# Performance work log

Hardware: AMD Instinct MI355X
Metric: run time of the kernel (lower is better)

The kernel has to match this reference:

```python
import jax, jax.numpy as jnp
import numpy as np

B, C, T, K = 16, 512, 2048, 64

def setup_inputs() -> dict:
    key = jax.random.key(0)
    k1, k2, k3 = jax.random.split(key, 3)
    v = jax.random.normal(k1, (B, C, T), dtype=jnp.float32)
    # 1x1 Conv1d weights == linear maps over channel dim
    Wk = jax.random.normal(k2, (K, C), dtype=jnp.float32) * 0.02
    bk = jnp.zeros((K,), dtype=jnp.float32)
    Wq = jax.random.normal(k3, (K, C), dtype=jnp.float32) * 0.02
    bq = jnp.zeros((K,), dtype=jnp.float32)
    gamma = jnp.ones((), dtype=jnp.float32)
    return {"v": v, "Wk": Wk, "bk": bk, "Wq": Wq, "bq": bq, "gamma": gamma}

def reference(v, Wk, bk, Wq, bq, gamma):
    # k, q: (B, K, T) via 1x1 conv = channel-wise linear
    k = jnp.einsum('kc,bct->bkt', Wk, v) + bk[None, :, None]
    q = jnp.einsum('kc,bct->bkt', Wq, v) + bq[None, :, None]
    # original: e1[b,d,i,j]=q[b,d,j], e2[b,d,i,j]=k[b,d,i]; sum over d
    # -> s[b,i,j] = sum_d k[b,d,i] * q[b,d,j]  (avoid materializing B,K,T,T)
    s = jnp.einsum('bdi,bdj->bij', k, q)  # (B, T, T)
    a = jax.nn.softmax(s, axis=1)          # softmax over dim=1 (the i axis)
    att = jnp.einsum('bct,btj->bcj', v, a)  # bmm(v, a)
    return v + gamma * att
```

## Files before the change

### kernel.cpp

```cpp
#include <hip/hip_runtime.h>

#define Bc 16
#define Cc 512
#define Tc 2048
#define QT 128
#define KT 64
#define NT 32
#define LTS 66

typedef __attribute__((ext_vector_type(8)))  short short8;
typedef __attribute__((ext_vector_type(4)))  float f32x4;
typedef __attribute__((ext_vector_type(16))) float f32x16;
typedef unsigned short u16;

static __device__ __forceinline__ u16 f2bf(float x) {
  unsigned u = __float_as_uint(x);
  u += 0x7FFF + ((u >> 16) & 1);
  return (u16)(u >> 16);
}

static __device__ __forceinline__ unsigned cvt_pk_bf16(float lo, float hi) {
  unsigned r;
  asm("v_cvt_pk_bf16_f32 %0, %1, %2" : "=v"(r) : "v"(lo), "v"(hi));
  return r;
}

static __device__ __forceinline__ void gload_lds16(const u16* gsrc, u16* ldst) {
  __builtin_amdgcn_global_load_lds(
      (const __attribute__((address_space(1))) unsigned int*)gsrc,
      (__attribute__((address_space(3))) unsigned int*)ldst,
      16, 0, 0);
}

static __device__ __forceinline__ void block_sync_lds() {
  __builtin_amdgcn_sched_barrier(0);
  asm volatile("s_waitcnt lgkmcnt(0)" ::: "memory");
  __builtin_amdgcn_s_barrier();
  __builtin_amdgcn_sched_barrier(0);
}

static __device__ __forceinline__ void block_sync_vm4() {
  __builtin_amdgcn_sched_barrier(0);
  asm volatile("s_waitcnt vmcnt(4) lgkmcnt(0)" ::: "memory");
  __builtin_amdgcn_s_barrier();
  __builtin_amdgcn_sched_barrier(0);
}

__global__ __launch_bounds__(256) void prep_kernel(
    const float* __restrict__ Wk, const float* __restrict__ Wq,
    const float* __restrict__ bk, const float* __restrict__ bq,
    u16* __restrict__ Wbf, float* __restrict__ bkq)
{
  int idx  = blockIdx.x * 256 + threadIdx.x;
  int base = idx * 4;
  if (base < 128 * Cc) {
    int ch = base >> 9;
    int c  = base & (Cc - 1);
    const float* src = (ch < 64) ? (Wk + (size_t)ch * Cc + c)
                                 : (Wq + (size_t)(ch - 64) * Cc + c);
    f32x4 w = *reinterpret_cast<const f32x4*>(src);
    uint2 o;
    o.x = (unsigned)f2bf(w[0]) | ((unsigned)f2bf(w[1]) << 16);
    o.y = (unsigned)f2bf(w[2]) | ((unsigned)f2bf(w[3]) << 16);
    *reinterpret_cast<uint2*>(Wbf + base) = o;
  }
  if (idx < 128) bkq[idx] = (idx < 64) ? bk[idx] : bq[idx - 64];
}

__global__ __launch_bounds__(256) void kqv_kernel(
    const float* __restrict__ v, const u16* __restrict__ Wbf,
    const float* __restrict__ bkq, u16* __restrict__ kq, u16* __restrict__ vbf)
{
  __shared__ u16 LDSt[2][64][LTS];
  const int b   = blockIdx.y;
  const int t0  = blockIdx.x * 64;
  const int tid = threadIdx.x;
  const int lane = tid & 63;
  const int w    = tid >> 6;
  const int l15  = lane & 15;
  const int lg   = lane >> 4;

  f32x4 acc[8];
  #pragma unroll
  for (int mt = 0; mt < 8; ++mt) acc[mt] = f32x4{0.f, 0.f, 0.f, 0.f};

  const float* vb = v + (size_t)b * Cc * Tc + t0;
  float x[16];
  #pragma unroll
  for (int r = 0; r < 16; ++r) x[r] = vb[(size_t)(w * 16 + r) * Tc + lane];

  int buf = 0;
  for (int c0 = 0; c0 < Cc; c0 += 64, buf ^= 1) {
    #pragma unroll
    for (int r = 0; r < 16; ++r) {
      u16 hb = f2bf(x[r]);
      LDSt[buf][lane][w * 16 + r] = hb;
      vbf[((size_t)b * Cc + c0 + w * 16 + r) * Tc + t0 + lane] = hb;
    }
    block_sync_lds();
    if (c0 + 64 < Cc) {
      #pragma unroll
      for (int r = 0; r < 16; ++r)
        x[r] = vb[(size_t)(c0 + 64 + w * 16 + r) * Tc + lane];
    }
    #pragma unroll
    for (int ks = 0; ks < 2; ++ks) {
      short8 bfrag = *reinterpret_cast<const short8*>(&LDSt[buf][w * 16 + l15][ks * 32 + lg * 8]);
      #pragma unroll
      for (int mt = 0; mt < 8; ++mt) {
        short8 afrag = *reinterpret_cast<const short8*>(
            Wbf + (size_t)(mt * 16 + l15) * Cc + c0 + ks * 32 + lg * 8);
        acc[mt] = __builtin_amdgcn_mfma_f32_16x16x32_bf16(afrag, bfrag, acc[mt], 0, 0, 0);
      }
    }
  }
  const int t = t0 + w * 16 + l15;
  u16* op = kq + ((size_t)b * Tc + t) * 128;
  #pragma unroll
  for (int mt = 0; mt < 8; ++mt) {
    int chb = mt * 16 + lg * 4;
    uint2 o;
    o.x = cvt_pk_bf16(acc[mt][0] + bkq[chb + 0], acc[mt][1] + bkq[chb + 1]);
    o.y = cvt_pk_bf16(acc[mt][2] + bkq[chb + 2], acc[mt][3] + bkq[chb + 3]);
    *reinterpret_cast<uint2*>(op + chb) = o;
  }
}

__global__ __launch_bounds__(512, 2) void attn_kernel(
    const float* __restrict__ v, const u16* __restrict__ vbf,
    const u16* __restrict__ kq, const float* __restrict__ gamma_p,
    float* __restrict__ out)
{
  __shared__ u16 P[2][128 * 64];
  __shared__ u16 Klds[2][64 * 64];
  __shared__ __align__(16) float ep_lds[8][32 * 36];
  __shared__ float lsum_lds[QT];
  __shared__ __align__(16) float linv_lds[QT];

  const int L   = blockIdx.x;
  const int lin = (L & 7) * 32 + (L >> 3);
  const int b   = lin >> 4;
  const int j0  = (lin & 15) * QT;
  const int tid = threadIdx.x;
  const int lane = tid & 63;
  const int wid  = tid >> 6;
  const int l15  = lane & 15;
  const int lg   = lane >> 4;
  const int l31  = lane & 31;
  const int kh   = lane >> 5;
  const int c0   = wid * 64;

  const int sr = wid * 8 + (lane >> 3);
  const int sc = (lane & 7) ^ ((lane >> 3) & 7);
  const u16* kqb2 = kq + (size_t)b * Tc * 128;
  u16* kst_dst = &Klds[0][0] + wid * 8 * 64;

  short8 qf0, qf1;
  {
    const u16* qp = kq + (size_t)(b * Tc + j0 + wid * 16 + l15) * 128 + 64 + lg * 8;
    qf0 = *reinterpret_cast<const short8*>(qp);
    qf1 = *reinterpret_cast<const short8*>(qp + 32);
  }

  f32x16 O32[2][4];
  #pragma unroll
  for (int a = 0; a < 2; ++a)
    #pragma unroll
    for (int bb = 0; bb < 4; ++bb)
      #pragma unroll
      for (int e = 0; e < 16; ++e) O32[a][bb][e] = 0.f;

  float lsum = 0.f;

  const u16* vbase = vbf + ((size_t)b * Cc + c0) * Tc;
  short8 vf0[2][2];

  gload_lds16(kqb2 + (size_t)sr * 128 + sc * 8, kst_dst + 0 * 4096);
  __syncthreads();
  {
    short8 kf[4][2];
    #pragma unroll
    for (int it = 0; it < 4; ++it)
      #pragma unroll
      for (int ks = 0; ks < 2; ++ks)
        kf[it][ks] = *reinterpret_cast<const short8*>(
            &Klds[0][(it * 16 + l15) * 64 + (((ks * 4 + lg) ^ (l15 & 7)) * 8)]);
    f32x4 sacc[4];
    #pragma unroll
    for (int it = 0; it < 4; ++it) {
      f32x4 s = f32x4{0.f, 0.f, 0.f, 0.f};
      s = __builtin_amdgcn_mfma_f32_16x16x32_bf16(kf[it][0], qf0, s, 0, 0, 0);
      s = __builtin_amdgcn_mfma_f32_16x16x32_bf16(kf[it][1], qf1, s, 0, 0, 0);
      sacc[it] = s;
    }
    u16* prow = &P[0][(wid * 16 + l15) * 64];
    #pragma unroll
    for (int it = 0; it < 4; ++it) {
      float p0 = __expf(sacc[it][0]);
      float p1 = __expf(sacc[it][1]);
      float p2 = __expf(sacc[it][2]);
      float p3 = __expf(sacc[it][3]);
      lsum += (p0 + p1) + (p2 + p3);
      uint2 wv;
      wv.x = cvt_pk_bf16(p0, p1);
      wv.y = cvt_pk_bf16(p2, p3);
      int chk = ((it * 2 + (lg >> 1)) ^ (l15 & 7)) * 8 + (lg & 1) * 4;
      *reinterpret_cast<uint2*>(prow + chk) = wv;
    }
  }
  gload_lds16(kqb2 + (size_t)(KT + sr) * 128 + sc * 8, kst_dst + 1 * 4096);
  #pragma unroll
  for (int ct = 0; ct < 2; ++ct)
    #pragma unroll
    for (int kk = 0; kk < 2; ++kk)
      vf0[ct][kk] = *reinterpret_cast<const short8*>(
          vbase + (size_t)(ct * 32 + l31) * Tc + kk * 16 + kh * 8);
  block_sync_vm4();

  int pb = 0;
  for (int i = 0; i < NT; ++i, pb ^= 1) {
    const int i0 = i * KT;
    const bool last = (i + 1 >= NT);

    short8 vf1[2][2];
    #pragma unroll
    for (int ct = 0; ct < 2; ++ct)
      #pragma unroll
      for (int kk = 0; kk < 2; ++kk)
        vf1[ct][kk] = *reinterpret_cast<const short8*>(
            vbase + (size_t)(ct * 32 + l31) * Tc + i0 + 32 + kk * 16 + kh * 8);

    if (i + 2 < NT)
      gload_lds16(kqb2 + (size_t)(i0 + 2 * KT + sr) * 128 + sc * 8,
                  kst_dst + (i & 1) * 4096);

    if (!last) {
      short8 kf[4][2];
      #pragma unroll
      for (int it = 0; it < 4; ++it)
        #pragma unroll
        for (int ks = 0; ks < 2; ++ks)
          kf[it][ks] = *reinterpret_cast<const short8*>(
              &Klds[(i + 1) & 1][(it * 16 + l15) * 64 + (((ks * 4 + lg) ^ (l15 & 7)) * 8)]);
      f32x4 sacc[4];
      #pragma unroll
      for (int it = 0; it < 4; ++it) {
        f32x4 s = f32x4{0.f, 0.f, 0.f, 0.f};
        s = __builtin_amdgcn_mfma_f32_16x16x32_bf16(kf[it][0], qf0, s, 0, 0, 0);
        s = __builtin_amdgcn_mfma_f32_16x16x32_bf16(kf[it][1], qf1, s, 0, 0, 0);
        sacc[it] = s;
      }
      u16* prow = &P[pb ^ 1][(wid * 16 + l15) * 64];
      #pragma unroll
      for (int it = 0; it < 4; ++it) {
        float p0 = __expf(sacc[it][0]);
        float p1 = __expf(sacc[it][1]);
        float p2 = __expf(sacc[it][2]);
        float p3 = __expf(sacc[it][3]);
        lsum += (p0 + p1) + (p2 + p3);
        uint2 wv;
        wv.x = cvt_pk_bf16(p0, p1);
        wv.y = cvt_pk_bf16(p2, p3);
        int chk = ((it * 2 + (lg >> 1)) ^ (l15 & 7)) * 8 + (lg & 1) * 4;
        *reinterpret_cast<uint2*>(prow + chk) = wv;
      }
    }

    #pragma unroll
    for (int ks = 0; ks < 4; ++ks) {
      short8 pf[4];
      #pragma unroll
      for (int jt = 0; jt < 4; ++jt) {
        int row = jt * 32 + l31;
        int chk = ((ks * 2 + kh) ^ (row & 7)) * 8;
        pf[jt] = *reinterpret_cast<const short8*>(&P[pb][row * 64 + chk]);
      }
      const short8* vsel0 = (ks < 2) ? &vf0[0][ks] : &vf1[0][ks - 2];
      const short8* vsel1 = (ks < 2) ? &vf0[1][ks] : &vf1[1][ks - 2];
      #pragma unroll
      for (int jt = 0; jt < 4; ++jt) {
        O32[0][jt] = __builtin_amdgcn_mfma_f32_32x32x16_bf16(*vsel0, pf[jt], O32[0][jt], 0, 0, 0);
        O32[1][jt] = __builtin_amdgcn_mfma_f32_32x32x16_bf16(*vsel1, pf[jt], O32[1][jt], 0, 0, 0);
      }
    }

    if (!last) {
      #pragma unroll
      for (int ct = 0; ct < 2; ++ct)
        #pragma unroll
        for (int kk = 0; kk < 2; ++kk)
          vf0[ct][kk] = *reinterpret_cast<const short8*>(
              vbase + (size_t)(ct * 32 + l31) * Tc + (i0 + KT) + kk * 16 + kh * 8);
      block_sync_vm4();
    }
  }

  lsum += __shfl_xor(lsum, 16);
  lsum += __shfl_xor(lsum, 32);
  if (lane < 16) lsum_lds[wid * 16 + lane] = lsum;
  __syncthreads();
  const float gamma = *gamma_p;
  if (tid < QT) linv_lds[tid] = gamma / lsum_lds[tid];
  __syncthreads();

  float* ep = ep_lds[wid];
  const int rd_row = lane >> 3;
  const int rd_ch  = lane & 7;
  #pragma unroll
  for (int ct = 0; ct < 2; ++ct) {
    #pragma unroll
    for (int jt = 0; jt < 4; ++jt) {
      #pragma unroll
      for (int reg = 0; reg < 16; ++reg) {
        int cl = (reg & 3) + 8 * (reg >> 2) + 4 * kh;
        ep[cl * 36 + l31] = O32[ct][jt][reg];
      }
      asm volatile("s_waitcnt lgkmcnt(0)" ::: "memory");
      __builtin_amdgcn_sched_barrier(0);
      #pragma unroll
      for (int h = 0; h < 4; ++h) {
        const int row = rd_row + 8 * h;
        f32x4 o4 = *reinterpret_cast<const f32x4*>(&ep[row * 36 + rd_ch * 4]);
        const int jg = jt * 32 + rd_ch * 4;
        f32x4 li = *reinterpret_cast<const f32x4*>(&linv_lds[jg]);
        const int c_glob = c0 + ct * 32 + row;
        const float* vr = v + ((size_t)(b * Cc + c_glob)) * Tc + j0 + jg;
        float* orow = out + ((size_t)(b * Cc + c_glob)) * Tc + j0 + jg;
        f32x4 v4 = *reinterpret_cast<const f32x4*>(vr);
        f32x4 o;
        o[0] = v4[0] + li[0] * o4[0];
        o[1] = v4[1] + li[1] * o4[1];
        o[2] = v4[2] + li[2] * o4[2];
        o[3] = v4[3] + li[3] * o4[3];
        *reinterpret_cast<f32x4*>(orow) = o;
      }
      asm volatile("s_waitcnt lgkmcnt(0)" ::: "memory");
      __builtin_amdgcn_sched_barrier(0);
    }
  }
}

extern "C" void kernel_launch(void* const* d_in, const int* in_sizes, int n_in,
                              void* d_out, int out_size, void* d_ws, size_t ws_size,
                              hipStream_t stream) {
  const float* v  = (const float*)d_in[0];
  const float* Wk = (const float*)d_in[1];
  const float* bk = (const float*)d_in[2];
  const float* Wq = (const float*)d_in[3];
  const float* bq = (const float*)d_in[4];
  const float* gm = (const float*)d_in[5];
  float* out = (float*)d_out;

  char* ws = (char*)d_ws;
  u16*   kqb = (u16*)ws;
  u16*   vbf = (u16*)(ws + 8388608);
  u16*   Wbf = (u16*)(ws + 8388608 + 33554432);
  float* bkq = (float*)(ws + 8388608 + 33554432 + 131072);

  prep_kernel<<<dim3(64), dim3(256), 0, stream>>>(Wk, Wq, bk, bq, Wbf, bkq);
  kqv_kernel<<<dim3(Tc / 64, Bc), dim3(256), 0, stream>>>(v, Wbf, bkq, kqb, vbf);
  attn_kernel<<<dim3((Tc / QT) * Bc), dim3(512), 0, stream>>>(v, vbf, kqb, gm, out);
}
```

Measured before the change: 157.2 us.

## Double key tile to 128 and pipeline V fragment loads across PV steps

Result: no change. 157.1 us (-0.1%).

```diff
diff --git a/kernel.cpp b/kernel.cpp
--- a/kernel.cpp
+++ b/kernel.cpp
@@ -4,8 +4,8 @@
 #define Cc 512
 #define Tc 2048
 #define QT 128
-#define KT 64
-#define NT 32
+#define KT 128
+#define NT 16
 #define LTS 66
 
 typedef __attribute__((ext_vector_type(8)))  short short8;
@@ -126,14 +126,40 @@
   }
 }
 
+#define VLOAD(VF, KSB, IB)                                                \
+  _Pragma("unroll")                                                       \
+  for (int ct_ = 0; ct_ < 2; ++ct_)                                       \
+    _Pragma("unroll")                                                     \
+    for (int kk_ = 0; kk_ < 2; ++kk_)                                     \
+      VF[ct_][kk_] = *reinterpret_cast<const short8*>(                    \
+          vbase + (size_t)(ct_ * 32 + l31) * Tc + (IB) + ((KSB) + kk_) * 16 + kh * 8);
+
+#define PVSTEP(VF, KSB)                                                   \
+  {                                                                       \
+    _Pragma("unroll")                                                     \
+    for (int kk_ = 0; kk_ < 2; ++kk_) {                                   \
+      short8 pf_[4];                                                      \
+      _Pragma("unroll")                                                   \
+      for (int jt_ = 0; jt_ < 4; ++jt_) {                                 \
+        int row_ = jt_ * 32 + l31;                                        \
+        int chk_ = ((((KSB) + kk_) * 2 + kh) ^ (row_ & 15)) * 8;          \
+        pf_[jt_] = *reinterpret_cast<const short8*>(&P[pb][row_ * 128 + chk_]); \
+      }                                                                   \
+      _Pragma("unroll")                                                   \
+      for (int jt_ = 0; jt_ < 4; ++jt_) {                                 \
+        O32[0][jt_] = __builtin_amdgcn_mfma_f32_32x32x16_bf16(VF[0][kk_], pf_[jt_], O32[0][jt_], 0, 0, 0); \
+        O32[1][jt_] = __builtin_amdgcn_mfma_f32_32x32x16_bf16(VF[1][kk_], pf_[jt_], O32[1][jt_], 0, 0, 0); \
+      }                                                                   \
+    }                                                                     \
+  }
+
 __global__ __launch_bounds__(512, 2) void attn_kernel(
     const float* __restrict__ v, const u16* __restrict__ vbf,
     const u16* __restrict__ kq, const float* __restrict__ gamma_p,
     float* __restrict__ out)
 {
-  __shared__ u16 P[2][128 * 64];
-  __shared__ u16 Klds[2][64 * 64];
-  __shared__ __align__(16) float ep_lds[8][32 * 36];
+  __shared__ u16 P[2][128 * 128];
+  __shared__ u16 Klds[2][128 * 64];
   __shared__ float lsum_lds[QT];
   __shared__ __align__(16) float linv_lds[QT];
 
@@ -150,10 +176,9 @@
   const int kh   = lane >> 5;
   const int c0   = wid * 64;
 
-  const int sr = wid * 8 + (lane >> 3);
   const int sc = (lane & 7) ^ ((lane >> 3) & 7);
   const u16* kqb2 = kq + (size_t)b * Tc * 128;
-  u16* kst_dst = &Klds[0][0] + wid * 8 * 64;
+  u16* kst = &Klds[0][0] + wid * 16 * 64;
 
   short8 qf0, qf1;
   {
@@ -173,48 +198,48 @@
   float lsum = 0.f;
 
   const u16* vbase = vbf + ((size_t)b * Cc + c0) * Tc;
-  short8 vf0[2][2];
-
-  gload_lds16(kqb2 + (size_t)sr * 128 + sc * 8, kst_dst + 0 * 4096);
+  short8 vfA[2][2], vfB[2][2];
+
+  gload_lds16(kqb2 + (size_t)(wid * 16 + (lane >> 3)) * 128 + sc * 8, kst);
+  gload_lds16(kqb2 + (size_t)(wid * 16 + 8 + (lane >> 3)) * 128 + sc * 8, kst + 8 * 64);
   __syncthreads();
   {
-    short8 kf[4][2];
-    #pragma unroll
-    for (int it = 0; it < 4; ++it)
-      #pragma unroll
-      for (int ks = 0; ks < 2; ++ks)
-        kf[it][ks] = *reinterpret_cast<const short8*>(
-            &Klds[0][(it * 16 + l15) * 64 + (((ks * 4 + lg) ^ (l15 & 7)) * 8)]);
-    f32x4 sacc[4];
-    #pragma unroll
-    for (int it = 0; it < 4; ++it) {
-      f32x4 s = f32x4{0.f, 0.f, 0.f, 0.f};
-      s = __builtin_amdgcn_mfma_f32_16x16x32_bf16(kf[it][0], qf0, s, 0, 0, 0);
-      s = __builtin_amdgcn_mfma_f32_16x16x32_bf16(kf[it][1], qf1, s, 0, 0, 0);
-      sacc[it] = s;
-    }
-    u16* prow = &P[0][(wid * 16 + l15) * 64];
-    #pragma unroll
-    for (int it = 0; it < 4; ++it) {
-      float p0 = __expf(sacc[it][0]);
-      float p1 = __expf(sacc[it][1]);
-      float p2 = __expf(sacc[it][2]);
-      float p3 = __expf(sacc[it][3]);
-      lsum += (p0 + p1) + (p2 + p3);
-      uint2 wv;
-      wv.x = cvt_pk_bf16(p0, p1);
-      wv.y = cvt_pk_bf16(p2, p3);
-      int chk = ((it * 2 + (lg >> 1)) ^ (l15 & 7)) * 8 + (lg & 1) * 4;
-      *reinterpret_cast<uint2*>(prow + chk) = wv;
-    }
-  }
-  gload_lds16(kqb2 + (size_t)(KT + sr) * 128 + sc * 8, kst_dst + 1 * 4096);
-  #pragma unroll
-  for (int ct = 0; ct < 2; ++ct)
-    #pragma unroll
-    for (int kk = 0; kk < 2; ++kk)
-      vf0[ct][kk] = *reinterpret_cast<const short8*>(
-          vbase + (size_t)(ct * 32 + l31) * Tc + kk * 16 + kh * 8);
+    u16* prow = &P[0][(wid * 16 + l15) * 128];
+    #pragma unroll
+    for (int hg = 0; hg < 2; ++hg) {
+      short8 kf[4][2];
+      #pragma unroll
+      for (int it2 = 0; it2 < 4; ++it2)
+        #pragma unroll
+        for (int ks = 0; ks < 2; ++ks)
+          kf[it2][ks] = *reinterpret_cast<const short8*>(
+              &Klds[0][((hg * 4 + it2) * 16 + l15) * 64 + (((ks * 4 + lg) ^ (l15 & 7)) * 8)]);
+      f32x4 sacc[4];
+      #pragma unroll
+      for (int it2 = 0; it2 < 4; ++it2) {
+        f32x4 s = f32x4{0.f, 0.f, 0.f, 0.f};
+        s = __builtin_amdgcn_mfma_f32_16x16x32_bf16(kf[it2][0], qf0, s, 0, 0, 0);
+        s = __builtin_amdgcn_mfma_f32_16x16x32_bf16(kf[it2][1], qf1, s, 0, 0, 0);
+        sacc[it2] = s;
+      }
+      #pragma unroll
+      for (int it2 = 0; it2 < 4; ++it2) {
+        float p0 = __expf(sacc[it2][0]);
+        float p1 = __expf(sacc[it2][1]);
+        float p2 = __expf(sacc[it2][2]);
+        float p3 = __expf(sacc[it2][3]);
+        lsum += (p0 + p1) + (p2 + p3);
+        uint2 wv;
+        wv.x = cvt_pk_bf16(p0, p1);
+        wv.y = cvt_pk_bf16(p2, p3);
+        int chk = ((hg * 8 + it2 * 2 + (lg >> 1)) ^ (l15 & 15)) * 8 + (lg & 1) * 4;
+        *reinterpret_cast<uint2*>(prow + chk) = wv;
+      }
+    }
+  }
+  gload_lds16(kqb2 + (size_t)(KT + wid * 16 + (lane >> 3)) * 128 + sc * 8, kst + 8192);
+  gload_lds16(kqb2 + (size_t)(KT + wid * 16 + 8 + (lane >> 3)) * 128 + sc * 8, kst + 8192 + 8 * 64);
+  VLOAD(vfA, 0, 0);
   block_sync_vm4();
 
   int pb = 0;
@@ -222,77 +247,61 @@
     const int i0 = i * KT;
     const bool last = (i + 1 >= NT);
 
-    short8 vf1[2][2];
-    #pragma unroll
-    for (int ct = 0; ct < 2; ++ct)
-      #pragma unroll
-      for (int kk = 0; kk < 2; ++kk)
-        vf1[ct][kk] = *reinterpret_cast<const short8*>(
-            vbase + (size_t)(ct * 32 + l31) * Tc + i0 + 32 + kk * 16 + kh * 8);
-
-    if (i + 2 < NT)
-      gload_lds16(kqb2 + (size_t)(i0 + 2 * KT + sr) * 128 + sc * 8,
-                  kst_dst + (i & 1) * 4096);
+    VLOAD(vfB, 2, i0);
+
+    if (i + 2 < NT) {
+      const size_t kb = (size_t)(i0 + 2 * KT);
+      gload_lds16(kqb2 + (kb + wid * 16 + (lane >> 3)) * 128 + sc * 8,
+                  kst + (i & 1) * 8192);
+      gload_lds16(kqb2 + (kb + wid * 16 + 8 + (lane >> 3)) * 128 + sc * 8,
+                  kst + (i & 1) * 8192 + 8 * 64);
+    }
 
     if (!last) {
-      short8 kf[4][2];
-      #pragma unroll
-      for (int it = 0; it < 4; ++it)
+      const u16* kl = &Klds[(i + 1) & 1][0];
+      u16* prow = &P[pb ^ 1][(wid * 16 + l15) * 128];
+      #pragma unroll
+      for (int hg = 0; hg < 2; ++hg) {
+        short8 kf[4][2];
         #pragma unroll
-        for (int ks = 0; ks < 2; ++ks)
-          kf[it][ks] = *reinterpret_cast<const short8*>(
-              &Klds[(i + 1) & 1][(it * 16 + l15) * 64 + (((ks * 4 + lg) ^ (l15 & 7)) * 8)]);
-      f32x4 sacc[4];
-      #pragma unroll
-      for (int it = 0; it < 4; ++it) {
-        f32x4 s = f32x4{0.f, 0.f, 0.f, 0.f};
-        s = __builtin_amdgcn_mfma_f32_16x16x32_bf16(kf[it][0], qf0, s, 0, 0, 0);
-        s = __builtin_amdgcn_mfma_f32_16x16x32_bf16(kf[it][1], qf1, s, 0, 0, 0);
-        sacc[it] = s;
-      }
-      u16* prow = &P[pb ^ 1][(wid * 16 + l15) * 64];
-      #pragma unroll
-      for (int it = 0; it < 4; ++it) {
-        float p0 = __expf(sacc[it][0]);
-        float p1 = __expf(sacc[it][1]);
-        float p2 = __expf(sacc[it][2]);
-        float p3 = __expf(sacc[it][3]);
-        lsum += (p0 + p1) + (p2 + p3);
-        uint2 wv;
-        wv.x = cvt_pk_bf16(p0, p1);
-        wv.y = cvt_pk_bf16(p2, p3);
-        int chk = ((it * 2 + (lg >> 1)) ^ (l15 & 7)) * 8 + (lg & 1) * 4;
-        *reinterpret_cast<uint2*>(prow + chk) = wv;
-      }
-    }
-
-    #pragma unroll
-    for (int ks = 0; ks < 4; ++ks) {
-      short8 pf[4];
-      #pragma unroll
-      for (int jt = 0; jt < 4; ++jt) {
-        int row = jt * 32 + l31;
-        int chk = ((ks * 2 + kh) ^ (row & 7)) * 8;
-        pf[jt] = *reinterpret_cast<const short8*>(&P[pb][row * 64 + chk]);
-      }
-      const short8* vsel0 = (ks < 2) ? &vf0[0][ks] : &vf1[0][ks - 2];
-      const short8* vsel1 = (ks < 2) ? &vf0[1][ks] : &vf1[1][ks - 2];
-      #pragma unroll
-      for (int jt = 0; jt < 4; ++jt) {
-        O32[0][jt] = __builtin_amdgcn_mfma_f32_32x32x16_bf16(*vsel0, pf[jt], O32[0][jt], 0, 0, 0);
-        O32[1][jt] = __builtin_amdgcn_mfma_f32_32x32x16_bf16(*vsel1, pf[jt], O32[1][jt], 0, 0, 0);
-      }
-    }
-
-    if (!last) {
-      #pragma unroll
-      for (int ct = 0; ct < 2; ++ct)
+        for (int it2 = 0; it2 < 4; ++it2)
+          #pragma unroll
+          for (int ks = 0; ks < 2; ++ks)
+            kf[it2][ks] = *reinterpret_cast<const short8*>(
+                &kl[((hg * 4 + it2) * 16 + l15) * 64 + (((ks * 4 + lg) ^ (l15 & 7)) * 8)]);
+        f32x4 sacc[4];
         #pragma unroll
-        for (int kk = 0; kk < 2; ++kk)
-          vf0[ct][kk] = *reinterpret_cast<const short8*>(
-              vbase + (size_t)(ct * 32 + l31) * Tc + (i0 + KT) + kk * 16 + kh * 8);
-      block_sync_vm4();
-    }
+        for (int it2 = 0; it2 < 4; ++it2) {
+          f32x4 s = f32x4{0.f, 0.f, 0.f, 0.f};
+          s = __builtin_amdgcn_mfma_f32_16x16x32_bf16(kf[it2][0], qf0, s, 0, 0, 0);
+          s = __builtin_amdgcn_mfma_f32_16x16x32_bf16(kf[it2][1], qf1, s, 0, 0, 0);
+          sacc[it2] = s;
+        }
+        #pragma unroll
+        for (int it2 = 0; it2 < 4; ++it2) {
+          float p0 = __expf(sacc[it2][0]);
+          float p1 = __expf(sacc[it2][1]);
+          float p2 = __expf(sacc[it2][2]);
+          float p3 = __expf(sacc[it2][3]);
+          lsum += (p0 + p1) + (p2 + p3);
+          uint2 wv;
+          wv.x = cvt_pk_bf16(p0, p1);
+          wv.y = cvt_pk_bf16(p2, p3);
+          int chk = ((hg * 8 + it2 * 2 + (lg >> 1)) ^ (l15 & 15)) * 8 + (lg & 1) * 4;
+          *reinterpret_cast<uint2*>(prow + chk) = wv;
+        }
+      }
+    }
+
+    PVSTEP(vfA, 0);
+    VLOAD(vfA, 4, i0);
+    PVSTEP(vfB, 2);
+    VLOAD(vfB, 6, i0);
+    PVSTEP(vfA, 4);
+    if (!last) VLOAD(vfA, 0, i0 + KT);
+    PVSTEP(vfB, 6);
+
+    if (!last) block_sync_vm4();
   }
 
   lsum += __shfl_xor(lsum, 16);
@@ -303,7 +312,7 @@
   if (tid < QT) linv_lds[tid] = gamma / lsum_lds[tid];
   __syncthreads();
 
-  float* ep = ep_lds[wid];
+  float* ep = reinterpret_cast<float*>(&P[0][0]) + wid * (32 * 36);
   const int rd_row = lane >> 3;
   const int rd_ch  = lane & 7;
   #pragma unroll
```
